# Kernel optimization log

Hardware: AMD Instinct MI355X
Metric: run time of the kernel (lower is better)

Reference implementation:

```python
import jax, jax.numpy as jnp
import numpy as np

K = 8  # K_num: neighbors per pred point


def setup_inputs() -> dict:
    key = jax.random.key(0)
    ks = jax.random.split(key, 8)
    B, Nr, Np, C = 2, 8192, 8192, 256
    s = 1.0 / np.sqrt(C)
    return {
        "xyz_ref": jax.random.normal(ks[0], (B, Nr, 3), jnp.float32) * 10.0,
        "xyz_pred": jax.random.normal(ks[1], (B, Np, 3), jnp.float32) * 10.0,
        "feat_k_ref": jax.random.normal(ks[2], (B, Nr, C), jnp.float32),
        "feat_q_pred": jax.random.normal(ks[3], (B, Np, C), jnp.float32),
        "feat_v_ref": jax.random.normal(ks[4], (B, Nr, C), jnp.float32),
        "Wv": jax.random.normal(ks[5], (C, C), jnp.float32) * s,
        "bv": jnp.zeros((C,), jnp.float32),
        "Wo": jax.random.normal(ks[6], (C, C), jnp.float32) * s,
        "bo": jnp.zeros((C,), jnp.float32),
        "Wout": jax.random.normal(ks[7], (2 * C, C), jnp.float32) * s,
    }


def reference(xyz_ref, xyz_pred, feat_k_ref, feat_q_pred, feat_v_ref, Wv, bv, Wo, bo, Wout):
    B, Np, C = feat_q_pred.shape
    Nr = feat_k_ref.shape[1]

    # --- KNN search (torch.no_grad in original) ---
    xr = jax.lax.stop_gradient(xyz_ref)
    xp = jax.lax.stop_gradient(xyz_pred)
    d2 = (jnp.sum(xp * xp, -1)[:, :, None]
          + jnp.sum(xr * xr, -1)[:, None, :]
          - 2.0 * jnp.einsum('bpd,brd->bpr', xp, xr))  # [B, Np, Nr]
    _, idx = jax.lax.top_k(-d2, K)  # [B, Np, K] nearest ref indices per pred point

    # --- W_v (Conv1d 1x1) applied to all ref values before gather ---
    v_all = jnp.einsum('brc,dc->brd', feat_v_ref, Wv) + bv  # [B, Nr, C]

    gather = jax.vmap(lambda f, i: f[i])  # per-sample fancy gather
    k = gather(feat_k_ref, idx)  # [B, Np, K, C]
    v = gather(v_all, idx)       # [B, Np, K, C]

    # --- tiny per-point cross attention over K neighbors ---
    scores = jnp.einsum('bpc,bpkc->bpk', feat_q_pred, k) / jnp.sqrt(jnp.asarray(C, feat_q_pred.dtype))
    attn = jax.nn.softmax(scores, axis=-1)          # [B, Np, K]
    out = jnp.einsum('bpk,bpkc->bpc', attn, v)      # [B, Np, C]

    # --- W_o (Conv1d 1x1) ---
    out = jnp.einsum('bpc,dc->bpd', out, Wo) + bo   # [B, Np, C]

    # --- scatter into full point set: ref rows stay zero, pred rows get out ---
    out_all = jnp.concatenate([jnp.zeros((B, Nr, C), out.dtype), out], axis=1)  # [B, Nr+Np, C]

    # --- W_out (MinkowskiConvolution k=1, no bias): C -> 2C ---
    return jnp.einsum('bnc,dc->bnd', out_all, Wout)  # [B, Nr+Np, 2C]
```

## Files before the change

### kernel.cpp

```cpp
#include <hip/hip_runtime.h>
#include <stdint.h>


#define NRr 8192
#define NPp 8192
#define NC  256
#define NK  8
#define NCH   16
#define CHUNK 512

typedef short bf16x8 __attribute__((ext_vector_type(8)));
typedef float f32x4  __attribute__((ext_vector_type(4)));

__device__ __forceinline__ uint16_t f2bf(float f) {
  uint32_t u = __float_as_uint(f);
  return (uint16_t)((u + 0x7fffu + ((u >> 16) & 1u)) >> 16);
}

__device__ __forceinline__ float d2f(float px, float py, float pz, float sp, float4 r) {
  float m0 = __fmul_rn(px, r.x), m1 = __fmul_rn(py, r.y), m2 = __fmul_rn(pz, r.z);
  float dot = __fadd_rn(__fadd_rn(m0, m1), m2);
  return __fsub_rn(__fadd_rn(sp, r.w), __fadd_rn(dot, dot));
}

__global__ __launch_bounds__(64) void k_prep(const float* __restrict__ xyz_ref,
                                             float4* __restrict__ ref4) {
  int i = blockIdx.x * 64 + threadIdx.x;
  if (i >= 2 * NRr) return;
  float x = xyz_ref[i*3+0];
  float y = xyz_ref[i*3+1];
  float z = xyz_ref[i*3+2];
  float n = __fadd_rn(__fadd_rn(__fmul_rn(x,x), __fmul_rn(y,y)), __fmul_rn(z,z));
  ref4[i] = make_float4(x, y, z, n);
}

__device__ __forceinline__ void insert8(float d2, int j, float (&dist)[8], int (&id)[8]) {
  if (d2 < dist[7]) {
    #pragma unroll
    for (int k = 7; k >= 1; --k) {
      bool sh = d2 < dist[k-1];
      bool pl = d2 < dist[k];
      float nd = sh ? dist[k-1] : (pl ? d2 : dist[k]);
      int   ni = sh ? id[k-1]   : (pl ? j  : id[k]);
      dist[k] = nd; id[k] = ni;
    }
    if (d2 < dist[0]) { dist[0] = d2; id[0] = j; }
  }
}

__global__ __launch_bounds__(256, 5) void k_knn(const float* __restrict__ xyz_pred,
                                                const float4* __restrict__ ref4,
                                                uint16_t* __restrict__ part,
                                                const float* __restrict__ Wv,
                                                const float* __restrict__ bv,
                                                const float* __restrict__ Wo,
                                                const float* __restrict__ bo,
                                                const float* __restrict__ Wout,
                                                uint16_t* __restrict__ Aw,
                                                float* __restrict__ bbig) {
  __shared__ __align__(16) char smem[32768];

  if (blockIdx.x < 64) {
    float (*M8)[256] = (float (*)[256])smem;
    float* red = (float*)(smem + 8192);
    int e0 = blockIdx.x * 8;
    int t  = threadIdx.x;

    float acc8[8];
    #pragma unroll
    for (int e = 0; e < 8; ++e) acc8[e] = 0.f;
    for (int d = 0; d < 256; ++d) {
      float wo = Wo[(size_t)d*256 + t];
      #pragma unroll
      for (int e = 0; e < 8; ++e)
        acc8[e] = fmaf(Wout[(size_t)(e0+e)*256 + d], wo, acc8[e]);
    }
    #pragma unroll
    for (int e = 0; e < 8; ++e) M8[e][t] = acc8[e];
    __syncthreads();

    float a8[8];
    #pragma unroll
    for (int e = 0; e < 8; ++e) a8[e] = 0.f;
    for (int c = 0; c < 256; ++c) {
      float wv = Wv[(size_t)c*256 + t];
      #pragma unroll
      for (int e = 0; e < 8; ++e)
        a8[e] = fmaf(M8[e][c], wv, a8[e]);
    }
    #pragma unroll
    for (int e = 0; e < 8; ++e) Aw[(size_t)(e0+e)*256 + t] = f2bf(a8[e]);

    for (int e = 0; e < 8; ++e) {
      red[t] = fmaf(M8[e][t], bv[t], Wout[(size_t)(e0+e)*256 + t] * bo[t]);
      __syncthreads();
      for (int s2 = 128; s2 > 0; s2 >>= 1) {
        if (t < s2) red[t] += red[t + s2];
        __syncthreads();
      }
      if (t == 0) bbig[e0+e] = red[0];
      __syncthreads();
    }
    return;
  }

  float4* sref = (float4*)smem;
  int wave = threadIdx.x >> 6;
  int lane = threadIdx.x & 63;
  int task = (blockIdx.x - 64) * 4 + wave;
  int ch   = task & (NCH - 1);
  int P    = (task >> 4) * 64 + lane;
  int b    = P >> 13;

  float px = xyz_pred[P*3+0];
  float py = xyz_pred[P*3+1];
  float pz = xyz_pred[P*3+2];
  float sp = __fadd_rn(__fadd_rn(__fmul_rn(px,px), __fmul_rn(py,py)), __fmul_rn(pz,pz));

  const float4* refbase = ref4 + (size_t)b * NRr;
  int rbase = ch * CHUNK;
  float4* srefw = sref + wave * CHUNK;
  for (int j = lane; j < CHUNK; j += 64) srefw[j] = refbase[rbase + j];

  float a0 = 3.4e38f, a1 = 3.4e38f, a2 = 3.4e38f, a3 = 3.4e38f;
  float g0 = 3.4e38f, g1 = 3.4e38f, g2 = 3.4e38f, g3 = 3.4e38f;
  float dist[8]; int id[8];
  #pragma unroll
  for (int k = 0; k < 8; ++k) { dist[k] = 3.4e38f; id[k] = 0; }

  for (int s = 0; s < CHUNK / 32; ++s) {
    uint32_t mm = 0;
    int base = s * 32;
    #pragma unroll 2
    for (int jj = 0; jj < 32; jj += 2) {
      float d0 = d2f(px, py, pz, sp, srefw[base + jj]);
      float d1 = d2f(px, py, pz, sp, srefw[base + jj + 1]);
      a3 = __builtin_amdgcn_fmed3f(d0, a2, a3);
      a2 = __builtin_amdgcn_fmed3f(d0, a1, a2);
      a1 = __builtin_amdgcn_fmed3f(d0, a0, a1);
      a0 = fminf(d0, a0);
      g3 = __builtin_amdgcn_fmed3f(d1, g2, g3);
      g2 = __builtin_amdgcn_fmed3f(d1, g1, g2);
      g1 = __builtin_amdgcn_fmed3f(d1, g0, g1);
      g0 = fminf(d1, g0);
      float tau = fmaxf(a3, g3);
      mm |= (uint32_t)(d0 <= tau) << jj;
      mm |= (uint32_t)(d1 <= tau) << (jj + 1);
    }
    while (mm) {
      int bit = __builtin_ctz(mm); mm &= mm - 1;
      int j = base + bit;
      float dd = d2f(px, py, pz, sp, srefw[j]);
      insert8(dd, j, dist, id);
    }
  }

  uint16_t* pp = part + ((size_t)P * NCH + ch) * 8;
  #pragma unroll
  for (int k = 0; k < 8; ++k)
    pp[k] = (uint16_t)((rbase + id[k]) & (NRr - 1));
}

__device__ __forceinline__ void insert_lex(float d2, int j, float (&dist)[8], int (&id)[8]) {
  bool b7 = (d2 < dist[7]) || (d2 == dist[7] && j < id[7]);
  if (b7) {
    #pragma unroll
    for (int k = 7; k >= 1; --k) {
      bool sh = (d2 < dist[k-1]) || (d2 == dist[k-1] && j < id[k-1]);
      bool pl = (d2 < dist[k])   || (d2 == dist[k]   && j < id[k]);
      float nd = sh ? dist[k-1] : (pl ? d2 : dist[k]);
      int   ni = sh ? id[k-1]   : (pl ? j  : id[k]);
      dist[k] = nd; id[k] = ni;
    }
    bool p0 = (d2 < dist[0]) || (d2 == dist[0] && j < id[0]);
    if (p0) { dist[0] = d2; id[0] = j; }
  }
}

__global__ __launch_bounds__(64) void k_merge(const uint16_t* __restrict__ part,
                                              const float* __restrict__ xyz_pred,
                                              const float4* __restrict__ ref4,
                                              int* __restrict__ idx) {
  int P = blockIdx.x * 64 + threadIdx.x;
  int b = P >> 13;
  float px = xyz_pred[P*3+0];
  float py = xyz_pred[P*3+1];
  float pz = xyz_pred[P*3+2];
  float sp = __fadd_rn(__fadd_rn(__fmul_rn(px,px), __fmul_rn(py,py)), __fmul_rn(pz,pz));
  const float4* refbase = ref4 + (size_t)b * NRr;

  float dist[8]; int id[8];
  #pragma unroll
  for (int k = 0; k < 8; ++k) { dist[k] = 3.4e38f; id[k] = NRr - 1; }

  const ushort4* pv = (const ushort4*)(part + (size_t)P * (NCH * 8));
  for (int c = 0; c < NCH * 2; ++c) {
    ushort4 v = pv[c];
    int j0 = v.x & (NRr - 1), j1 = v.y & (NRr - 1);
    int j2 = v.z & (NRr - 1), j3 = v.w & (NRr - 1);
    insert_lex(d2f(px, py, pz, sp, refbase[j0]), j0, dist, id);
    insert_lex(d2f(px, py, pz, sp, refbase[j1]), j1, dist, id);
    insert_lex(d2f(px, py, pz, sp, refbase[j2]), j2, dist, id);
    insert_lex(d2f(px, py, pz, sp, refbase[j3]), j3, dist, id);
  }
  #pragma unroll
  for (int k = 0; k < 8; ++k) idx[(size_t)P*8 + k] = id[k] & (NRr - 1);
}

__global__ __launch_bounds__(256) void k_attn(const float* __restrict__ feat_q,
    const float* __restrict__ feat_k, const float* __restrict__ feat_v,
    const int* __restrict__ idx, uint16_t* __restrict__ g) {
  int wave = threadIdx.x >> 6;
  int lane = threadIdx.x & 63;
  int P = blockIdx.x * 4 + wave;
  int b = P >> 13;
  const int* ip = idx + (size_t)P * 8;
  int nb[8];
  #pragma unroll
  for (int k = 0; k < 8; ++k) nb[k] = ip[k] & (NRr - 1);

  float4 qv = *(const float4*)(feat_q + (size_t)P*NC + lane*4);
  const float* kb = feat_k + (size_t)b * NRr * NC;
  const float* vb = feat_v + (size_t)b * NRr * NC;

  float s[8];
  #pragma unroll
  for (int k = 0; k < 8; ++k) {
    float4 kv = *(const float4*)(kb + (size_t)nb[k]*NC + lane*4);
    float p = qv.x * kv.x;
    p = fmaf(qv.y, kv.y, p);
    p = fmaf(qv.z, kv.z, p);
    p = fmaf(qv.w, kv.w, p);
    s[k] = p;
  }
  #pragma unroll
  for (int k = 0; k < 8; ++k) {
    float v = s[k];
    #pragma unroll
    for (int m = 1; m < 64; m <<= 1) v += __shfl_xor(v, m, 64);
    s[k] = v * 0.0625f;
  }
  float mx = s[0];
  #pragma unroll
  for (int k = 1; k < 8; ++k) mx = fmaxf(mx, s[k]);
  float e[8], sum = 0.f;
  #pragma unroll
  for (int k = 0; k < 8; ++k) { e[k] = expf(s[k] - mx); sum += e[k]; }
  float inv = 1.0f / sum;

  float g0 = 0.f, g1 = 0.f, g2 = 0.f, g3 = 0.f;
  #pragma unroll
  for (int k = 0; k < 8; ++k) {
    float4 vv = *(const float4*)(vb + (size_t)nb[k]*NC + lane*4);
    float w = e[k] * inv;
    g0 = fmaf(w, vv.x, g0);
    g1 = fmaf(w, vv.y, g1);
    g2 = fmaf(w, vv.z, g2);
    g3 = fmaf(w, vv.w, g3);
  }
  uint32_t p0 = ((uint32_t)f2bf(g1) << 16) | f2bf(g0);
  uint32_t p1 = ((uint32_t)f2bf(g3) << 16) | f2bf(g2);
  *(uint2*)(g + (size_t)P*NC + lane*4) = make_uint2(p0, p1);
}

__global__ void k_zero(float4* __restrict__ o) {
  int i = blockIdx.x * 256 + threadIdx.x;
  int b = i >> 20;
  int r = i & 1048575;
  o[(size_t)b * 2097152 + r] = make_float4(0.f, 0.f, 0.f, 0.f);
}

__global__ __launch_bounds__(256) void k_gemm(const uint16_t* __restrict__ g,
    const uint16_t* __restrict__ Aw, const float* __restrict__ bbig,
    float* __restrict__ outp) {
  __shared__ __align__(16) uint16_t sA[64 * 136];
  __shared__ __align__(16) uint16_t sB[64 * 136];
  int t = threadIdx.x;
  int lane = t & 63, wave = t >> 6;
  int wm = (wave >> 1) * 32, wn = (wave & 1) * 32;
  int q = lane >> 4, rr = lane & 15;
  int bm = blockIdx.x;
  int bn = blockIdx.y;
  f32x4 zero = {0.f, 0.f, 0.f, 0.f};
  f32x4 acc[2][2] = {{zero, zero}, {zero, zero}};

  for (int ph = 0; ph < 2; ++ph) {
    #pragma unroll
    for (int i = 0; i < 4; ++i) {
      int cc  = t + i * 256;
      int row = cc >> 4;
      int col = (cc & 15) << 3;
      uint4 da = *(const uint4*)(g  + ((size_t)(bm*64 + row))*NC + ph*128 + col);
      *(uint4*)(&sA[row*136 + col]) = da;
      uint4 db = *(const uint4*)(Aw + ((size_t)(bn*64 + row))*NC + ph*128 + col);
      *(uint4*)(&sB[row*136 + col]) = db;
    }
    __syncthreads();
    #pragma unroll
    for (int kk = 0; kk < 4; ++kk) {
      int ko = kk*32 + q*8;
      bf16x8 a0 = *(const bf16x8*)(&sA[(wm      + rr)*136 + ko]);
      bf16x8 a1 = *(const bf16x8*)(&sA[(wm + 16 + rr)*136 + ko]);
      bf16x8 b0 = *(const bf16x8*)(&sB[(wn      + rr)*136 + ko]);
      bf16x8 b1 = *(const bf16x8*)(&sB[(wn + 16 + rr)*136 + ko]);
      acc[0][0] = __builtin_amdgcn_mfma_f32_16x16x32_bf16(a0, b0, acc[0][0], 0, 0, 0);
      acc[0][1] = __builtin_amdgcn_mfma_f32_16x16x32_bf16(a0, b1, acc[0][1], 0, 0, 0);
      acc[1][0] = __builtin_amdgcn_mfma_f32_16x16x32_bf16(a1, b0, acc[1][0], 0, 0, 0);
      acc[1][1] = __builtin_amdgcn_mfma_f32_16x16x32_bf16(a1, b1, acc[1][1], 0, 0, 0);
    }
    __syncthreads();
  }
  #pragma unroll
  for (int j = 0; j < 2; ++j) {
    int col = bn*64 + wn + j*16 + rr;
    float bias = bbig[col];
    #pragma unroll
    for (int i = 0; i < 2; ++i) {
      #pragma unroll
      for (int r = 0; r < 4; ++r) {
        int row = bm*64 + wm + i*16 + q*4 + r;
        float v = acc[i][j][r] + bias;
        int bb = row >> 13, p = row & 8191;
        outp[((size_t)(bb*16384 + 8192 + p))*512 + col] = v;
      }
    }
  }
}

extern "C" void kernel_launch(void* const* d_in, const int* in_sizes, int n_in,
                              void* d_out, int out_size, void* d_ws, size_t ws_size,
                              hipStream_t stream) {
  const float* xyz_ref  = (const float*)d_in[0];
  const float* xyz_pred = (const float*)d_in[1];
  const float* feat_k   = (const float*)d_in[2];
  const float* feat_q   = (const float*)d_in[3];
  const float* feat_v   = (const float*)d_in[4];
  const float* Wv       = (const float*)d_in[5];
  const float* bv       = (const float*)d_in[6];
  const float* Wo       = (const float*)d_in[7];
  const float* bo       = (const float*)d_in[8];
  const float* Wout     = (const float*)d_in[9];
  float* outp = (float*)d_out;

  char* ob = (char*)d_out;
  uint16_t* g    = (uint16_t*)ob;
  float4*   ref4 = (float4*)(ob + 8388608);
  int*      idx  = (int*)(ob + 8650752);
  uint16_t* Aw   = (uint16_t*)(ob + 9175040);
  float*    bbig = (float*)(ob + 9437184);
  uint16_t* part = (uint16_t*)(ob + 33554432);

  k_prep   <<<256,  64,  0, stream>>>(xyz_ref, ref4);
  k_knn    <<<1088, 256, 0, stream>>>(xyz_pred, ref4, part,
                                      Wv, bv, Wo, bo, Wout, Aw, bbig);
  k_merge  <<<256,  64,  0, stream>>>(part, xyz_pred, ref4, idx);
  k_attn   <<<4096, 256, 0, stream>>>(feat_q, feat_k, feat_v, idx, g);
  k_gemm   <<<dim3(256, 8), 256, 0, stream>>>(g, Aw, bbig, outp);
  k_zero   <<<8192, 256, 0, stream>>>((float4*)outp);
}
```

Measured before the change: 353.7 us.

## Fuse top-k merge into attention kernel with wave-parallel shuffle reduction

```diff
diff --git a/kernel.cpp b/kernel.cpp
--- a/kernel.cpp
+++ b/kernel.cpp
@@ -21,6 +21,11 @@
   float m0 = __fmul_rn(px, r.x), m1 = __fmul_rn(py, r.y), m2 = __fmul_rn(pz, r.z);
   float dot = __fadd_rn(__fadd_rn(m0, m1), m2);
   return __fsub_rn(__fadd_rn(sp, r.w), __fadd_rn(dot, dot));
+}
+
+__device__ __forceinline__ uint32_t fkey(float f) {
+  uint32_t b = __float_as_uint(f);
+  return (b & 0x80000000u) ? ~b : (b | 0x80000000u);
 }
 
 __global__ __launch_bounds__(64) void k_prep(const float* __restrict__ xyz_ref,
@@ -161,63 +166,43 @@
     pp[k] = (uint16_t)((rbase + id[k]) & (NRr - 1));
 }
 
-__device__ __forceinline__ void insert_lex(float d2, int j, float (&dist)[8], int (&id)[8]) {
-  bool b7 = (d2 < dist[7]) || (d2 == dist[7] && j < id[7]);
-  if (b7) {
-    #pragma unroll
-    for (int k = 7; k >= 1; --k) {
-      bool sh = (d2 < dist[k-1]) || (d2 == dist[k-1] && j < id[k-1]);
-      bool pl = (d2 < dist[k])   || (d2 == dist[k]   && j < id[k]);
-      float nd = sh ? dist[k-1] : (pl ? d2 : dist[k]);
-      int   ni = sh ? id[k-1]   : (pl ? j  : id[k]);
-      dist[k] = nd; id[k] = ni;
-    }
-    bool p0 = (d2 < dist[0]) || (d2 == dist[0] && j < id[0]);
-    if (p0) { dist[0] = d2; id[0] = j; }
-  }
-}
-
-__global__ __launch_bounds__(64) void k_merge(const uint16_t* __restrict__ part,
-                                              const float* __restrict__ xyz_pred,
-                                              const float4* __restrict__ ref4,
-                                              int* __restrict__ idx) {
-  int P = blockIdx.x * 64 + threadIdx.x;
+__global__ __launch_bounds__(256) void k_attn(const float* __restrict__ feat_q,
+    const float* __restrict__ feat_k, const float* __restrict__ feat_v,
+    const uint16_t* __restrict__ part, const float* __restrict__ xyz_pred,
+    const float4* __restrict__ ref4, uint16_t* __restrict__ g) {
+  int wave = threadIdx.x >> 6;
+  int lane = threadIdx.x & 63;
+  int P = blockIdx.x * 4 + wave;
   int b = P >> 13;
+
   float px = xyz_pred[P*3+0];
   float py = xyz_pred[P*3+1];
   float pz = xyz_pred[P*3+2];
   float sp = __fadd_rn(__fadd_rn(__fmul_rn(px,px), __fmul_rn(py,py)), __fmul_rn(pz,pz));
   const float4* refbase = ref4 + (size_t)b * NRr;
 
-  float dist[8]; int id[8];
-  #pragma unroll
-  for (int k = 0; k < 8; ++k) { dist[k] = 3.4e38f; id[k] = NRr - 1; }
-
-  const ushort4* pv = (const ushort4*)(part + (size_t)P * (NCH * 8));
-  for (int c = 0; c < NCH * 2; ++c) {
-    ushort4 v = pv[c];
-    int j0 = v.x & (NRr - 1), j1 = v.y & (NRr - 1);
-    int j2 = v.z & (NRr - 1), j3 = v.w & (NRr - 1);
-    insert_lex(d2f(px, py, pz, sp, refbase[j0]), j0, dist, id);
-    insert_lex(d2f(px, py, pz, sp, refbase[j1]), j1, dist, id);
-    insert_lex(d2f(px, py, pz, sp, refbase[j2]), j2, dist, id);
-    insert_lex(d2f(px, py, pz, sp, refbase[j3]), j3, dist, id);
-  }
-  #pragma unroll
-  for (int k = 0; k < 8; ++k) idx[(size_t)P*8 + k] = id[k] & (NRr - 1);
-}
-
-__global__ __launch_bounds__(256) void k_attn(const float* __restrict__ feat_q,
-    const float* __restrict__ feat_k, const float* __restrict__ feat_v,
-    const int* __restrict__ idx, uint16_t* __restrict__ g) {
-  int wave = threadIdx.x >> 6;
-  int lane = threadIdx.x & 63;
-  int P = blockIdx.x * 4 + wave;
-  int b = P >> 13;
-  const int* ip = idx + (size_t)P * 8;
+  const uint32_t* pw = (const uint32_t*)(part + (size_t)P * (NCH * 8));
+  uint32_t two = pw[lane];
+  int j0 = two & (NRr - 1);
+  int j1 = (two >> 16) & (NRr - 1);
+  float d0 = d2f(px, py, pz, sp, refbase[j0]);
+  float d1 = d2f(px, py, pz, sp, refbase[j1]);
+  uint64_t k0 = ((uint64_t)fkey(d0) << 32) | (uint32_t)j0;
+  uint64_t k1 = ((uint64_t)fkey(d1) << 32) | (uint32_t)j1;
+
   int nb[8];
   #pragma unroll
-  for (int k = 0; k < 8; ++k) nb[k] = ip[k] & (NRr - 1);
+  for (int r = 0; r < 8; ++r) {
+    uint64_t m = (k0 < k1) ? k0 : k1;
+    #pragma unroll
+    for (int s = 1; s < 64; s <<= 1) {
+      uint64_t o = __shfl_xor(m, s, 64);
+      m = (o < m) ? o : m;
+    }
+    nb[r] = (int)(uint32_t)(m & 0xFFFFFFFFu) & (NRr - 1);
+    if (k0 == m) k0 = ~0ULL;
+    if (k1 == m) k1 = ~0ULL;
+  }
 
   float4 qv = *(const float4*)(feat_q + (size_t)P*NC + lane*4);
   const float* kb = feat_k + (size_t)b * NRr * NC;
@@ -345,7 +330,6 @@
   char* ob = (char*)d_out;
   uint16_t* g    = (uint16_t*)ob;
   float4*   ref4 = (float4*)(ob + 8388608);
-  int*      idx  = (int*)(ob + 8650752);
   uint16_t* Aw   = (uint16_t*)(ob + 9175040);
   float*    bbig = (float*)(ob + 9437184);
   uint16_t* part = (uint16_t*)(ob + 33554432);
@@ -353,8 +337,8 @@
   k_prep   <<<256,  64,  0, stream>>>(xyz_ref, ref4);
   k_knn    <<<1088, 256, 0, stream>>>(xyz_pred, ref4, part,
                                       Wv, bv, Wo, bo, Wout, Aw, bbig);
-  k_merge  <<<256,  64,  0, stream>>>(part, xyz_pred, ref4, idx);
-  k_attn   <<<4096, 256, 0, stream>>>(feat_q, feat_k, feat_v, idx, g);
+  k_attn   <<<4096, 256, 0, stream>>>(feat_q, feat_k, feat_v, part,
+                                      xyz_pred, ref4, g);
   k_gemm   <<<dim3(256, 8), 256, 0, stream>>>(g, Aw, bbig, outp);
   k_zero   <<<8192, 256, 0, stream>>>((float4*)outp);
 }
```

Result: faster. 292.3 us (-17.4%).
